# Performance work log

Measured on AMD Instinct MI355X. Metric: run time of the kernel, lower is better.

The kernel has to match this reference:

```python
import jax, jax.numpy as jnp
import numpy as np

B, M, D, S, TOPK = 8, 4096, 512, 128, 64


def setup_inputs() -> dict:
    key = jax.random.key(0)
    ks = jax.random.split(key, 9)
    return {
        "memory": jax.random.normal(ks[0], (B, M, D), jnp.float32),
        "usage": jax.random.uniform(ks[1], (B, M), dtype=jnp.float32),
        "content": jax.random.normal(ks[2], (B, D), jnp.float32),
        "write_strength": jax.random.uniform(ks[3], (B, 1), dtype=jnp.float32),
        "query": jax.random.normal(ks[4], (B, S, D), jnp.float32),
        "key_proj_w": jax.random.normal(ks[5], (D, D), jnp.float32) * 0.02,
        "temporal_table": jax.random.normal(ks[6], (M, D), jnp.float32) * 0.02,
        "usage_decay": jnp.float32(0.99),
        "valid_mask": jax.random.randint(ks[7], (B, M), 0, 2) > 0,
        "write_index": jax.random.randint(ks[8], (B,), 0, M),
        "top_k": TOPK,
    }


def reference(memory, usage, content, write_strength, query, key_proj_w,
              temporal_table, usage_decay, valid_mask, write_index, top_k):
    # ---- write(): soft scatter into the slot selected by write_index ----
    idx = write_index % M                               # [B]
    temporal_emb = temporal_table[idx]                  # [B, D] gather
    content_wt = content + temporal_emb                 # [B, D]
    write_pos = jax.nn.one_hot(idx, M, dtype=memory.dtype)      # [B, M]
    a = write_pos[:, :, None] * write_strength[:, :, None]      # [B, M, 1]
    memory = memory * (1.0 - a) + content_wt[:, None, :] * a    # [B, M, D]
    valid = jnp.logical_or(valid_mask, write_pos > 0)           # [B, M]
    usage = usage * usage_decay + write_pos * write_strength    # [B, M]
    # ---- read(): content-based addressing with top-k masked softmax ----
    keys = jnp.einsum("bmd,ed->bme", memory, key_proj_w)        # Linear, no bias
    scores = jnp.einsum("bsd,bmd->bsm", query, keys) / (D ** 0.5)
    scores = jnp.where(valid[:, None, :], scores, -jnp.inf)
    top_vals = jax.lax.top_k(scores, top_k)[0]                  # [B, S, top_k]
    threshold = top_vals[..., -1:]                              # kth value
    scores = jnp.where(scores < threshold, -jnp.inf, scores)
    attn = jax.nn.softmax(scores, axis=-1)                      # [B, S, M]
    all_invalid = jnp.all(~valid, axis=-1)[:, None, None]
    attn = jnp.where(all_invalid, 0.0, attn)
    retrieved = jnp.einsum("bsm,bmd->bsd", attn, memory)        # [B, S, D]
    return retrieved, attn, usage
```

## Files before the change

### kernel.cpp

```cpp
#include <hip/hip_runtime.h>
#include <hip/hip_bf16.h>
#include <math.h>

#define BB 8
#define MM 4096
#define DD 512
#define SS 128

typedef short s16x8 __attribute__((ext_vector_type(8)));
typedef float f32x4 __attribute__((ext_vector_type(4)));

__device__ __forceinline__ unsigned short f2bf(float x) {
  unsigned u = __float_as_uint(x);
  unsigned r = u + 0x7fffu + ((u >> 16) & 1u);
  return (unsigned short)(r >> 16);
}
__device__ __forceinline__ float bf2f(unsigned short h) {
  return __uint_as_float(((unsigned)h) << 16);
}
__device__ __forceinline__ void split3(float x, unsigned short& s1,
                                       unsigned short& s2, unsigned short& s3) {
  s1 = f2bf(x);
  float r1 = x - bf2f(s1);
  s2 = f2bf(r1);
  float r2 = r1 - bf2f(s2);
  s3 = f2bf(r2);
}

__global__ __launch_bounds__(256) void update_kernel(
    float* __restrict__ memory, const float* __restrict__ usage,
    const float* __restrict__ content, const float* __restrict__ wstr,
    const float* __restrict__ ttab, const float* __restrict__ decay_p,
    const int* __restrict__ widx, float* __restrict__ usage_out) {
  const int b = blockIdx.x;
  int idx = widx[b] % MM; if (idx < 0) idx += MM;
  const float ws = wstr[b];
  const float decay = decay_p[0];
  for (int d = threadIdx.x; d < DD; d += blockDim.x) {
    float cw = content[b * DD + d] + ttab[(size_t)idx * DD + d];
    size_t off = (size_t)b * MM * DD + (size_t)idx * DD + d;
    float old = memory[off];
    memory[off] = old * (1.0f - ws) + cw * ws;
  }
  for (int m = threadIdx.x; m < MM; m += blockDim.x) {
    float u = usage[b * MM + m] * decay;
    if (m == idx) u += ws;
    usage_out[b * MM + m] = u;
  }
}

#define BMq 64
#define BNq 64
#define BKq 32
#define PADq 4

__global__ __launch_bounds__(256) void gemm_nn_qp(
    const float* __restrict__ A, const float* __restrict__ Bw,
    unsigned short* __restrict__ q1, unsigned short* __restrict__ q2,
    unsigned short* __restrict__ q3) {
  __shared__ __align__(16) float As[BKq][BMq + PADq];
  __shared__ __align__(16) float Bs[BKq][BNq + PADq];
  const int tid = threadIdx.x;
  const int tx = tid & 15, ty = tid >> 4;
  const int i0 = blockIdx.y * BMq;
  const int j0 = blockIdx.x * BNq;
  float acc[4][4] = {{0.f}};
  for (int k0 = 0; k0 < DD; k0 += BKq) {
#pragma unroll
    for (int r = 0; r < 2; ++r) {
      int ff = tid + r * 256;
      int row = ff >> 3, kq = ff & 7;
      float4 v = *(const float4*)(A + (size_t)(i0 + row) * DD + k0 + kq * 4);
      As[kq * 4 + 0][row] = v.x; As[kq * 4 + 1][row] = v.y;
      As[kq * 4 + 2][row] = v.z; As[kq * 4 + 3][row] = v.w;
      int kr = ff >> 4, jq = ff & 15;
      float4 w = *(const float4*)(Bw + (size_t)(k0 + kr) * DD + j0 + jq * 4);
      *(float4*)&Bs[kr][jq * 4] = w;
    }
    __syncthreads();
#pragma unroll
    for (int k = 0; k < BKq; ++k) {
      float4 a = *(const float4*)&As[k][ty * 4];
      float4 bb = *(const float4*)&Bs[k][tx * 4];
      float av[4] = {a.x, a.y, a.z, a.w};
      float bv[4] = {bb.x, bb.y, bb.z, bb.w};
#pragma unroll
      for (int i = 0; i < 4; ++i)
#pragma unroll
        for (int j = 0; j < 4; ++j) acc[i][j] += av[i] * bv[j];
    }
    __syncthreads();
  }
#pragma unroll
  for (int i = 0; i < 4; ++i) {
    int row = i0 + ty * 4 + i;
    ushort4 v1, v2, v3;
    split3(acc[i][0], v1.x, v2.x, v3.x);
    split3(acc[i][1], v1.y, v2.y, v3.y);
    split3(acc[i][2], v1.z, v2.z, v3.z);
    split3(acc[i][3], v1.w, v2.w, v3.w);
    *(ushort4*)(q1 + (size_t)row * DD + j0 + tx * 4) = v1;
    *(ushort4*)(q2 + (size_t)row * DD + j0 + tx * 4) = v2;
    *(ushort4*)(q3 + (size_t)row * DD + j0 + tx * 4) = v3;
  }
}

#define LSTR 40

__global__ __launch_bounds__(256, 1) void gemm_scores_mfma(
    const unsigned short* __restrict__ q1_g,
    const unsigned short* __restrict__ q2_g,
    const unsigned short* __restrict__ q3_g,
    const float* __restrict__ mem, float* __restrict__ sc_out) {
  __shared__ __align__(16) unsigned short q1_s[128 * LSTR];
  __shared__ __align__(16) unsigned short q2_s[128 * LSTR];
  __shared__ __align__(16) unsigned short q3_s[128 * LSTR];
  __shared__ __align__(16) unsigned short m1_s[128 * LSTR];
  __shared__ __align__(16) unsigned short m2_s[128 * LSTR];
  __shared__ __align__(16) unsigned short m3_s[128 * LSTR];
  const int tid = threadIdx.x;
  const int b = blockIdx.x & 7;
  const int j0 = (blockIdx.x >> 3) * 128;
  const int wv = tid >> 6, lane = tid & 63;
  const int quad = lane >> 4, r = lane & 15;

  const int qrow0 = tid >> 2, qc = tid & 3;
  const int qrow1 = 64 + (tid >> 2);
  const unsigned short* q1b = q1_g + (size_t)b * SS * DD;
  const unsigned short* q2b = q2_g + (size_t)b * SS * DD;
  const unsigned short* q3b = q3_g + (size_t)b * SS * DD;
  const int mrow = tid >> 3, mk = tid & 7;
  const float* mbase = mem + ((size_t)b * MM + j0) * DD;

  f32x4 acc[2][8];
#pragma unroll
  for (int i = 0; i < 2; ++i)
#pragma unroll
    for (int j = 0; j < 8; ++j)
#pragma unroll
      for (int c = 0; c < 4; ++c) acc[i][j][c] = 0.f;

  uint4 q1r0, q1r1, q2r0, q2r1, q3r0, q3r1;
  float4 mr[4];

  q1r0 = *(const uint4*)(q1b + (size_t)qrow0 * DD + qc * 8);
  q1r1 = *(const uint4*)(q1b + (size_t)qrow1 * DD + qc * 8);
  q2r0 = *(const uint4*)(q2b + (size_t)qrow0 * DD + qc * 8);
  q2r1 = *(const uint4*)(q2b + (size_t)qrow1 * DD + qc * 8);
  q3r0 = *(const uint4*)(q3b + (size_t)qrow0 * DD + qc * 8);
  q3r1 = *(const uint4*)(q3b + (size_t)qrow1 * DD + qc * 8);
#pragma unroll
  for (int i = 0; i < 4; ++i)
    mr[i] = *(const float4*)(mbase + (size_t)(mrow + 32 * i) * DD + mk * 4);

  for (int ks = 0; ks < 16; ++ks) {
    if (ks) __syncthreads();
    *(uint4*)&q1_s[qrow0 * LSTR + qc * 8] = q1r0;
    *(uint4*)&q1_s[qrow1 * LSTR + qc * 8] = q1r1;
    *(uint4*)&q2_s[qrow0 * LSTR + qc * 8] = q2r0;
    *(uint4*)&q2_s[qrow1 * LSTR + qc * 8] = q2r1;
    *(uint4*)&q3_s[qrow0 * LSTR + qc * 8] = q3r0;
    *(uint4*)&q3_s[qrow1 * LSTR + qc * 8] = q3r1;
#pragma unroll
    for (int i = 0; i < 4; ++i) {
      ushort4 v1, v2, v3;
      split3(mr[i].x, v1.x, v2.x, v3.x);
      split3(mr[i].y, v1.y, v2.y, v3.y);
      split3(mr[i].z, v1.z, v2.z, v3.z);
      split3(mr[i].w, v1.w, v2.w, v3.w);
      int row = mrow + 32 * i;
      *(ushort4*)&m1_s[row * LSTR + mk * 4] = v1;
      *(ushort4*)&m2_s[row * LSTR + mk * 4] = v2;
      *(ushort4*)&m3_s[row * LSTR + mk * 4] = v3;
    }
    __syncthreads();
    if (ks < 15) {
      int k0 = (ks + 1) * 32;
      q1r0 = *(const uint4*)(q1b + (size_t)qrow0 * DD + k0 + qc * 8);
      q1r1 = *(const uint4*)(q1b + (size_t)qrow1 * DD + k0 + qc * 8);
      q2r0 = *(const uint4*)(q2b + (size_t)qrow0 * DD + k0 + qc * 8);
      q2r1 = *(const uint4*)(q2b + (size_t)qrow1 * DD + k0 + qc * 8);
      q3r0 = *(const uint4*)(q3b + (size_t)qrow0 * DD + k0 + qc * 8);
      q3r1 = *(const uint4*)(q3b + (size_t)qrow1 * DD + k0 + qc * 8);
#pragma unroll
      for (int i = 0; i < 4; ++i)
        mr[i] = *(const float4*)(mbase + (size_t)(mrow + 32 * i) * DD + k0 + mk * 4);
    }
    s16x8 a1[2], a2[2], a3[2];
#pragma unroll
    for (int st = 0; st < 2; ++st) {
      int arow = wv * 32 + st * 16 + r;
      a1[st] = *(const s16x8*)&q1_s[arow * LSTR + quad * 8];
      a2[st] = *(const s16x8*)&q2_s[arow * LSTR + quad * 8];
      a3[st] = *(const s16x8*)&q3_s[arow * LSTR + quad * 8];
    }
#pragma unroll
    for (int jt = 0; jt < 8; ++jt) {
      int brow = jt * 16 + r;
      s16x8 b1 = *(const s16x8*)&m1_s[brow * LSTR + quad * 8];
      s16x8 b2 = *(const s16x8*)&m2_s[brow * LSTR + quad * 8];
      s16x8 b3 = *(const s16x8*)&m3_s[brow * LSTR + quad * 8];
#pragma unroll
      for (int st = 0; st < 2; ++st) {
        acc[st][jt] = __builtin_amdgcn_mfma_f32_16x16x32_bf16(a1[st], b3, acc[st][jt], 0, 0, 0);
        acc[st][jt] = __builtin_amdgcn_mfma_f32_16x16x32_bf16(a3[st], b1, acc[st][jt], 0, 0, 0);
        acc[st][jt] = __builtin_amdgcn_mfma_f32_16x16x32_bf16(a2[st], b2, acc[st][jt], 0, 0, 0);
        acc[st][jt] = __builtin_amdgcn_mfma_f32_16x16x32_bf16(a1[st], b2, acc[st][jt], 0, 0, 0);
        acc[st][jt] = __builtin_amdgcn_mfma_f32_16x16x32_bf16(a2[st], b1, acc[st][jt], 0, 0, 0);
        acc[st][jt] = __builtin_amdgcn_mfma_f32_16x16x32_bf16(a1[st], b1, acc[st][jt], 0, 0, 0);
      }
    }
  }
  const float scl = 0.04419417382415922f;
  float* C = sc_out + (size_t)b * SS * MM;
#pragma unroll
  for (int st = 0; st < 2; ++st)
#pragma unroll
    for (int jt = 0; jt < 8; ++jt)
#pragma unroll
      for (int reg = 0; reg < 4; ++reg) {
        int srow = wv * 32 + st * 16 + quad * 4 + reg;
        int scol = j0 + jt * 16 + r;
        C[(size_t)srow * MM + scol] = acc[st][jt][reg] * scl;
      }
}

__device__ __forceinline__ unsigned fkey(float f) {
  unsigned u = __float_as_uint(f);
  return (u & 0x80000000u) ? ~u : (u | 0x80000000u);
}
__device__ __forceinline__ float finv(unsigned u) {
  unsigned b = (u & 0x80000000u) ? (u & 0x7fffffffu) : ~u;
  return __uint_as_float(b);
}

__global__ __launch_bounds__(256) void select_kernel(
    const float* __restrict__ scores, const int* __restrict__ vmask,
    const int* __restrict__ widx, const int* __restrict__ topk,
    const float* __restrict__ memory, float* __restrict__ retrieved,
    float* __restrict__ attn) {
  __shared__ float sc[MM];
  __shared__ int kept[MM];
  __shared__ unsigned histw[4 * 256];
  __shared__ float red[256];
  __shared__ unsigned sh_pref;
  __shared__ int sh_k, sh_nkept;
  __shared__ float sh_zinv;

  const int tid = threadIdx.x;
  const int s = blockIdx.x, b = blockIdx.y;
  int wi = widx[b] % MM; if (wi < 0) wi += MM;
  const float4* srow4 = (const float4*)(scores + ((size_t)b * SS + s) * MM);
  const int4* vrow4 = (const int4*)(vmask + (size_t)b * MM);
  unsigned* hw = histw + (tid >> 6) * 256;

  if (tid == 0) { sh_pref = 0u; sh_nkept = 0; sh_k = topk[0]; }
  for (int i = tid; i < 1024; i += 256) histw[i] = 0u;
  __syncthreads();

  float lmax = -INFINITY;
  for (int m4 = tid; m4 < MM / 4; m4 += 256) {
    float4 v = srow4[m4];
    int4 mk = vrow4[m4];
    int mb = m4 * 4;
    if (!(mk.x || mb + 0 == wi)) v.x = -INFINITY;
    if (!(mk.y || mb + 1 == wi)) v.y = -INFINITY;
    if (!(mk.z || mb + 2 == wi)) v.z = -INFINITY;
    if (!(mk.w || mb + 3 == wi)) v.w = -INFINITY;
    ((float4*)sc)[m4] = v;
    lmax = fmaxf(lmax, fmaxf(fmaxf(v.x, v.y), fmaxf(v.z, v.w)));
    atomicAdd(&hw[fkey(v.x) >> 24], 1u);
    atomicAdd(&hw[fkey(v.y) >> 24], 1u);
    atomicAdd(&hw[fkey(v.z) >> 24], 1u);
    atomicAdd(&hw[fkey(v.w) >> 24], 1u);
  }
  red[tid] = lmax;
  __syncthreads();
#pragma unroll
  for (int off = 128; off > 0; off >>= 1) {
    if (tid < off) red[tid] = fmaxf(red[tid], red[tid + off]);
    __syncthreads();
  }
  const float maxv = red[0];

  for (int pass = 0; pass < 4; ++pass) {
    const int shift = 24 - pass * 8;
    if (pass > 0) {
      const unsigned pref = sh_pref;
      const unsigned hmask = 0xFFFFFFFFu << (shift + 8);
      for (int i = tid; i < 1024; i += 256) histw[i] = 0u;
      __syncthreads();
      for (int m = tid; m < MM; m += 256) {
        unsigned u = fkey(sc[m]);
        if ((u & hmask) == pref) atomicAdd(&hw[(u >> shift) & 0xFFu], 1u);
      }
      __syncthreads();
    }
    if (tid < 64) {
      const int l = tid;
      unsigned h0 = histw[l * 4 + 0] + histw[256 + l * 4 + 0] + histw[512 + l * 4 + 0] + histw[768 + l * 4 + 0];
      unsigned h1 = histw[l * 4 + 1] + histw[256 + l * 4 + 1] + histw[512 + l * 4 + 1] + histw[768 + l * 4 + 1];
      unsigned h2 = histw[l * 4 + 2] + histw[256 + l * 4 + 2] + histw[512 + l * 4 + 2] + histw[768 + l * 4 + 2];
      unsigned h3 = histw[l * 4 + 3] + histw[256 + l * 4 + 3] + histw[512 + l * 4 + 3] + histw[768 + l * 4 + 3];
      unsigned lsum = h0 + h1 + h2 + h3;
      unsigned g = lsum;
#pragma unroll
      for (int off = 1; off < 64; off <<= 1) {
        unsigned t = __shfl_down(g, off, 64);
        if (l + off < 64) g += t;
      }
      unsigned above = g - lsum;
      unsigned suf3 = h3 + above;
      unsigned suf2 = h2 + suf3;
      unsigned suf1 = h1 + suf2;
      unsigned suf0 = h0 + suf1;
      const unsigned kk = (unsigned)sh_k;
      const unsigned prefc = sh_pref;
      unsigned ge, geN;
      ge = suf0; geN = suf1;
      if (ge >= kk && geN < kk) { sh_pref = prefc | ((unsigned)(4 * l + 0) << shift); sh_k = (int)(kk - geN); }
      ge = suf1; geN = suf2;
      if (ge >= kk && geN < kk) { sh_pref = prefc | ((unsigned)(4 * l + 1) << shift); sh_k = (int)(kk - geN); }
      ge = suf2; geN = suf3;
      if (ge >= kk && geN < kk) { sh_pref = prefc | ((unsigned)(4 * l + 2) << shift); sh_k = (int)(kk - geN); }
      ge = suf3; geN = above;
      if (ge >= kk && geN < kk) { sh_pref = prefc | ((unsigned)(4 * l + 3) << shift); sh_k = (int)(kk - geN); }
    }
    __syncthreads();
  }
  const float thr = finv(sh_pref);

  float lz = 0.f;
  for (int m4 = tid; m4 < MM / 4; m4 += 256) {
    float4 v = ((float4*)sc)[m4];
    v.x = (v.x >= thr) ? __expf(v.x - maxv) : 0.f;
    v.y = (v.y >= thr) ? __expf(v.y - maxv) : 0.f;
    v.z = (v.z >= thr) ? __expf(v.z - maxv) : 0.f;
    v.w = (v.w >= thr) ? __expf(v.w - maxv) : 0.f;
    ((float4*)sc)[m4] = v;
    lz += v.x + v.y + v.z + v.w;
  }
  red[tid] = lz;
  __syncthreads();
#pragma unroll
  for (int off = 128; off > 0; off >>= 1) {
    if (tid < off) red[tid] += red[tid + off];
    __syncthreads();
  }
  if (tid == 0) sh_zinv = 1.0f / red[0];
  __syncthreads();
  const float zinv = sh_zinv;

  float4* arow4 = (float4*)(attn + ((size_t)b * SS + s) * MM);
  for (int m4 = tid; m4 < MM / 4; m4 += 256) {
    float4 p = ((float4*)sc)[m4];
    float4 o = make_float4(p.x * zinv, p.y * zinv, p.z * zinv, p.w * zinv);
    arow4[m4] = o;
    int mb = m4 * 4;
    if (p.x > 0.f) kept[atomicAdd(&sh_nkept, 1)] = mb + 0;
    if (p.y > 0.f) kept[atomicAdd(&sh_nkept, 1)] = mb + 1;
    if (p.z > 0.f) kept[atomicAdd(&sh_nkept, 1)] = mb + 2;
    if (p.w > 0.f) kept[atomicAdd(&sh_nkept, 1)] = mb + 3;
  }
  __syncthreads();
  const int nk = sh_nkept;

  float a0 = 0.f, a1 = 0.f;
  const float* mb_ = memory + (size_t)b * MM * DD;
  int i = 0;
  for (; i + 4 <= nk; i += 4) {
    int m0 = kept[i], m1 = kept[i + 1], m2 = kept[i + 2], m3 = kept[i + 3];
    float p0 = sc[m0], p1 = sc[m1], p2 = sc[m2], p3 = sc[m3];
    const float* r0 = mb_ + (size_t)m0 * DD;
    const float* r1 = mb_ + (size_t)m1 * DD;
    const float* r2 = mb_ + (size_t)m2 * DD;
    const float* r3 = mb_ + (size_t)m3 * DD;
    float v0a = r0[tid], v0b = r0[tid + 256];
    float v1a = r1[tid], v1b = r1[tid + 256];
    float v2a = r2[tid], v2b = r2[tid + 256];
    float v3a = r3[tid], v3b = r3[tid + 256];
    a0 += p0 * v0a + p1 * v1a + p2 * v2a + p3 * v3a;
    a1 += p0 * v0b + p1 * v1b + p2 * v2b + p3 * v3b;
  }
  for (; i < nk; ++i) {
    int m = kept[i];
    float p = sc[m];
    const float* mr = mb_ + (size_t)m * DD;
    a0 += p * mr[tid];
    a1 += p * mr[tid + 256];
  }
  float* rrow = retrieved + ((size_t)b * SS + s) * DD;
  rrow[tid] = a0 * zinv;
  rrow[tid + 256] = a1 * zinv;
}

extern "C" void kernel_launch(void* const* d_in, const int* in_sizes, int n_in,
                              void* d_out, int out_size, void* d_ws,
                              size_t ws_size, hipStream_t stream) {
  float* memory = (float*)d_in[0];
  const float* usage = (const float*)d_in[1];
  const float* content = (const float*)d_in[2];
  const float* wstr = (const float*)d_in[3];
  const float* query = (const float*)d_in[4];
  const float* W = (const float*)d_in[5];
  const float* ttab = (const float*)d_in[6];
  const float* decay = (const float*)d_in[7];
  const int* vmask = (const int*)d_in[8];
  const int* widx = (const int*)d_in[9];
  const int* topk = (const int*)d_in[10];

  float* out = (float*)d_out;
  float* retrieved = out;
  float* attn = out + (size_t)BB * SS * DD;
  float* usage_out = attn + (size_t)BB * SS * MM;

  const size_t qsz = (size_t)BB * SS * DD;
  float* scores = (float*)d_ws;
  unsigned short* q1 = (unsigned short*)(scores + (size_t)BB * SS * MM);
  unsigned short* q2 = q1 + qsz;
  unsigned short* q3;
  size_t need3 = (size_t)BB * SS * MM * 4 + 3 * qsz * 2;
  if (ws_size >= need3) {
    q3 = q2 + qsz;
  } else {
    q3 = (unsigned short*)(attn + (size_t)BB * SS * MM) - qsz;
  }

  update_kernel<<<BB, 256, 0, stream>>>(memory, usage, content, wstr, ttab,
                                        decay, widx, usage_out);
  gemm_nn_qp<<<dim3(DD / BNq, (BB * SS) / BMq), 256, 0, stream>>>(query, W, q1,
                                                                  q2, q3);
  gemm_scores_mfma<<<dim3((MM / 128) * BB), 256, 0, stream>>>(q1, q2, q3,
                                                              memory, scores);
  select_kernel<<<dim3(SS, BB), 256, 0, stream>>>(scores, vmask, widx, topk,
                                                  memory, retrieved, attn);
}
```

Before: 203.4 us.

## Switch split-precision GEMMs from 3-way bf16 to 2-way fp16 MFMA

Replaces the 3-term bf16 split (6 MFMAs per tile) with a 2-term fp16 hi/lo split (3 MFMAs) in the scores GEMM. The query-projection GEMM moves from scalar FP32 FMA to fp16 MFMA with the same split. The scores kernel now uses 64-column tiles, reads query fragments straight from global memory into registers instead of staging them in LDS, and allows two blocks per CU. This cuts MFMA count and LDS traffic, but fp16 has a narrower exponent range and coarser split precision, which could perturb the top-k ordering.

```diff
diff --git a/kernel.cpp b/kernel.cpp
--- a/kernel.cpp
+++ b/kernel.cpp
@@ -7,24 +7,17 @@
 #define DD 512
 #define SS 128
 
-typedef short s16x8 __attribute__((ext_vector_type(8)));
+typedef _Float16 f16;
+typedef _Float16 f16x4 __attribute__((ext_vector_type(4)));
+typedef _Float16 f16x8 __attribute__((ext_vector_type(8)));
 typedef float f32x4 __attribute__((ext_vector_type(4)));
 
-__device__ __forceinline__ unsigned short f2bf(float x) {
-  unsigned u = __float_as_uint(x);
-  unsigned r = u + 0x7fffu + ((u >> 16) & 1u);
-  return (unsigned short)(r >> 16);
-}
-__device__ __forceinline__ float bf2f(unsigned short h) {
-  return __uint_as_float(((unsigned)h) << 16);
-}
-__device__ __forceinline__ void split3(float x, unsigned short& s1,
-                                       unsigned short& s2, unsigned short& s3) {
-  s1 = f2bf(x);
-  float r1 = x - bf2f(s1);
-  s2 = f2bf(r1);
-  float r2 = r1 - bf2f(s2);
-  s3 = f2bf(r2);
+struct f16pair { f16 h; f16 l; };
+__device__ __forceinline__ f16pair split2(float x) {
+  f16pair p;
+  p.h = (f16)x;
+  p.l = (f16)(x - (float)p.h);
+  return p;
 }
 
 __global__ __launch_bounds__(256) void update_kernel(
@@ -49,166 +42,197 @@
   }
 }
 
-#define BMq 64
-#define BNq 64
-#define BKq 32
-#define PADq 4
-
-__global__ __launch_bounds__(256) void gemm_nn_qp(
-    const float* __restrict__ A, const float* __restrict__ Bw,
-    unsigned short* __restrict__ q1, unsigned short* __restrict__ q2,
-    unsigned short* __restrict__ q3) {
-  __shared__ __align__(16) float As[BKq][BMq + PADq];
-  __shared__ __align__(16) float Bs[BKq][BNq + PADq];
+#define QLSTR 40
+
+__global__ __launch_bounds__(256) void gemm_qp_mfma(
+    const float* __restrict__ query, const float* __restrict__ W,
+    f16* __restrict__ q1, f16* __restrict__ q2) {
+  __shared__ __align__(16) f16 A1s[64 * QLSTR];
+  __shared__ __align__(16) f16 A2s[64 * QLSTR];
+  __shared__ __align__(16) f16 B1s[64 * QLSTR];
+  __shared__ __align__(16) f16 B2s[64 * QLSTR];
   const int tid = threadIdx.x;
-  const int tx = tid & 15, ty = tid >> 4;
-  const int i0 = blockIdx.y * BMq;
-  const int j0 = blockIdx.x * BNq;
-  float acc[4][4] = {{0.f}};
-  for (int k0 = 0; k0 < DD; k0 += BKq) {
-#pragma unroll
-    for (int r = 0; r < 2; ++r) {
-      int ff = tid + r * 256;
-      int row = ff >> 3, kq = ff & 7;
-      float4 v = *(const float4*)(A + (size_t)(i0 + row) * DD + k0 + kq * 4);
-      As[kq * 4 + 0][row] = v.x; As[kq * 4 + 1][row] = v.y;
-      As[kq * 4 + 2][row] = v.z; As[kq * 4 + 3][row] = v.w;
-      int kr = ff >> 4, jq = ff & 15;
-      float4 w = *(const float4*)(Bw + (size_t)(k0 + kr) * DD + j0 + jq * 4);
-      *(float4*)&Bs[kr][jq * 4] = w;
-    }
-    __syncthreads();
-#pragma unroll
-    for (int k = 0; k < BKq; ++k) {
-      float4 a = *(const float4*)&As[k][ty * 4];
-      float4 bb = *(const float4*)&Bs[k][tx * 4];
-      float av[4] = {a.x, a.y, a.z, a.w};
-      float bv[4] = {bb.x, bb.y, bb.z, bb.w};
-#pragma unroll
-      for (int i = 0; i < 4; ++i)
-#pragma unroll
-        for (int j = 0; j < 4; ++j) acc[i][j] += av[i] * bv[j];
-    }
-    __syncthreads();
-  }
-#pragma unroll
-  for (int i = 0; i < 4; ++i) {
-    int row = i0 + ty * 4 + i;
-    ushort4 v1, v2, v3;
-    split3(acc[i][0], v1.x, v2.x, v3.x);
-    split3(acc[i][1], v1.y, v2.y, v3.y);
-    split3(acc[i][2], v1.z, v2.z, v3.z);
-    split3(acc[i][3], v1.w, v2.w, v3.w);
-    *(ushort4*)(q1 + (size_t)row * DD + j0 + tx * 4) = v1;
-    *(ushort4*)(q2 + (size_t)row * DD + j0 + tx * 4) = v2;
-    *(ushort4*)(q3 + (size_t)row * DD + j0 + tx * 4) = v3;
-  }
-}
-
-#define LSTR 40
-
-__global__ __launch_bounds__(256, 1) void gemm_scores_mfma(
-    const unsigned short* __restrict__ q1_g,
-    const unsigned short* __restrict__ q2_g,
-    const unsigned short* __restrict__ q3_g,
-    const float* __restrict__ mem, float* __restrict__ sc_out) {
-  __shared__ __align__(16) unsigned short q1_s[128 * LSTR];
-  __shared__ __align__(16) unsigned short q2_s[128 * LSTR];
-  __shared__ __align__(16) unsigned short q3_s[128 * LSTR];
-  __shared__ __align__(16) unsigned short m1_s[128 * LSTR];
-  __shared__ __align__(16) unsigned short m2_s[128 * LSTR];
-  __shared__ __align__(16) unsigned short m3_s[128 * LSTR];
-  const int tid = threadIdx.x;
-  const int b = blockIdx.x & 7;
-  const int j0 = (blockIdx.x >> 3) * 128;
+  const int n0 = blockIdx.x * 64;
+  const int r0 = blockIdx.y * 64;
   const int wv = tid >> 6, lane = tid & 63;
-  const int quad = lane >> 4, r = lane & 15;
-
-  const int qrow0 = tid >> 2, qc = tid & 3;
-  const int qrow1 = 64 + (tid >> 2);
-  const unsigned short* q1b = q1_g + (size_t)b * SS * DD;
-  const unsigned short* q2b = q2_g + (size_t)b * SS * DD;
-  const unsigned short* q3b = q3_g + (size_t)b * SS * DD;
-  const int mrow = tid >> 3, mk = tid & 7;
-  const float* mbase = mem + ((size_t)b * MM + j0) * DD;
-
-  f32x4 acc[2][8];
+  const int quad = lane >> 4, rr = lane & 15;
+  const int wr = wv & 1, wc = wv >> 1;
+
+  const int arow = tid >> 3, ak = tid & 7;
+  const int bkr = tid >> 4, bnq = tid & 15;
+
+  f32x4 acc[2][2];
 #pragma unroll
   for (int i = 0; i < 2; ++i)
 #pragma unroll
-    for (int j = 0; j < 8; ++j)
+    for (int j = 0; j < 2; ++j)
 #pragma unroll
       for (int c = 0; c < 4; ++c) acc[i][j][c] = 0.f;
 
-  uint4 q1r0, q1r1, q2r0, q2r1, q3r0, q3r1;
-  float4 mr[4];
-
-  q1r0 = *(const uint4*)(q1b + (size_t)qrow0 * DD + qc * 8);
-  q1r1 = *(const uint4*)(q1b + (size_t)qrow1 * DD + qc * 8);
-  q2r0 = *(const uint4*)(q2b + (size_t)qrow0 * DD + qc * 8);
-  q2r1 = *(const uint4*)(q2b + (size_t)qrow1 * DD + qc * 8);
-  q3r0 = *(const uint4*)(q3b + (size_t)qrow0 * DD + qc * 8);
-  q3r1 = *(const uint4*)(q3b + (size_t)qrow1 * DD + qc * 8);
-#pragma unroll
-  for (int i = 0; i < 4; ++i)
-    mr[i] = *(const float4*)(mbase + (size_t)(mrow + 32 * i) * DD + mk * 4);
+  float4 ar0, ar1, br0, br1;
+  ar0 = *(const float4*)(query + (size_t)(r0 + arow) * DD + ak * 4);
+  ar1 = *(const float4*)(query + (size_t)(r0 + arow + 32) * DD + ak * 4);
+  br0 = *(const float4*)(W + (size_t)bkr * DD + n0 + bnq * 4);
+  br1 = *(const float4*)(W + (size_t)(bkr + 16) * DD + n0 + bnq * 4);
 
   for (int ks = 0; ks < 16; ++ks) {
     if (ks) __syncthreads();
-    *(uint4*)&q1_s[qrow0 * LSTR + qc * 8] = q1r0;
-    *(uint4*)&q1_s[qrow1 * LSTR + qc * 8] = q1r1;
-    *(uint4*)&q2_s[qrow0 * LSTR + qc * 8] = q2r0;
-    *(uint4*)&q2_s[qrow1 * LSTR + qc * 8] = q2r1;
-    *(uint4*)&q3_s[qrow0 * LSTR + qc * 8] = q3r0;
-    *(uint4*)&q3_s[qrow1 * LSTR + qc * 8] = q3r1;
-#pragma unroll
-    for (int i = 0; i < 4; ++i) {
-      ushort4 v1, v2, v3;
-      split3(mr[i].x, v1.x, v2.x, v3.x);
-      split3(mr[i].y, v1.y, v2.y, v3.y);
-      split3(mr[i].z, v1.z, v2.z, v3.z);
-      split3(mr[i].w, v1.w, v2.w, v3.w);
-      int row = mrow + 32 * i;
-      *(ushort4*)&m1_s[row * LSTR + mk * 4] = v1;
-      *(ushort4*)&m2_s[row * LSTR + mk * 4] = v2;
-      *(ushort4*)&m3_s[row * LSTR + mk * 4] = v3;
+    {
+      f16x4 h, l;
+      f16pair p;
+      p = split2(ar0.x); h[0] = p.h; l[0] = p.l;
+      p = split2(ar0.y); h[1] = p.h; l[1] = p.l;
+      p = split2(ar0.z); h[2] = p.h; l[2] = p.l;
+      p = split2(ar0.w); h[3] = p.h; l[3] = p.l;
+      *(f16x4*)&A1s[arow * QLSTR + ak * 4] = h;
+      *(f16x4*)&A2s[arow * QLSTR + ak * 4] = l;
+      p = split2(ar1.x); h[0] = p.h; l[0] = p.l;
+      p = split2(ar1.y); h[1] = p.h; l[1] = p.l;
+      p = split2(ar1.z); h[2] = p.h; l[2] = p.l;
+      p = split2(ar1.w); h[3] = p.h; l[3] = p.l;
+      *(f16x4*)&A1s[(arow + 32) * QLSTR + ak * 4] = h;
+      *(f16x4*)&A2s[(arow + 32) * QLSTR + ak * 4] = l;
+      float wv4[4] = {br0.x, br0.y, br0.z, br0.w};
+#pragma unroll
+      for (int i = 0; i < 4; ++i) {
+        f16pair q = split2(wv4[i]);
+        B1s[(bnq * 4 + i) * QLSTR + bkr] = q.h;
+        B2s[(bnq * 4 + i) * QLSTR + bkr] = q.l;
+      }
+      float wv5[4] = {br1.x, br1.y, br1.z, br1.w};
+#pragma unroll
+      for (int i = 0; i < 4; ++i) {
+        f16pair q = split2(wv5[i]);
+        B1s[(bnq * 4 + i) * QLSTR + bkr + 16] = q.h;
+        B2s[(bnq * 4 + i) * QLSTR + bkr + 16] = q.l;
+      }
     }
     __syncthreads();
     if (ks < 15) {
       int k0 = (ks + 1) * 32;
-      q1r0 = *(const uint4*)(q1b + (size_t)qrow0 * DD + k0 + qc * 8);
-      q1r1 = *(const uint4*)(q1b + (size_t)qrow1 * DD + k0 + qc * 8);
-      q2r0 = *(const uint4*)(q2b + (size_t)qrow0 * DD + k0 + qc * 8);
-      q2r1 = *(const uint4*)(q2b + (size_t)qrow1 * DD + k0 + qc * 8);
-      q3r0 = *(const uint4*)(q3b + (size_t)qrow0 * DD + k0 + qc * 8);
-      q3r1 = *(const uint4*)(q3b + (size_t)qrow1 * DD + k0 + qc * 8);
-#pragma unroll
-      for (int i = 0; i < 4; ++i)
-        mr[i] = *(const float4*)(mbase + (size_t)(mrow + 32 * i) * DD + k0 + mk * 4);
-    }
-    s16x8 a1[2], a2[2], a3[2];
+      ar0 = *(const float4*)(query + (size_t)(r0 + arow) * DD + k0 + ak * 4);
+      ar1 = *(const float4*)(query + (size_t)(r0 + arow + 32) * DD + k0 + ak * 4);
+      br0 = *(const float4*)(W + (size_t)(k0 + bkr) * DD + n0 + bnq * 4);
+      br1 = *(const float4*)(W + (size_t)(k0 + bkr + 16) * DD + n0 + bnq * 4);
+    }
+    f16x8 a1[2], a2[2];
 #pragma unroll
     for (int st = 0; st < 2; ++st) {
-      int arow = wv * 32 + st * 16 + r;
-      a1[st] = *(const s16x8*)&q1_s[arow * LSTR + quad * 8];
-      a2[st] = *(const s16x8*)&q2_s[arow * LSTR + quad * 8];
-      a3[st] = *(const s16x8*)&q3_s[arow * LSTR + quad * 8];
-    }
-#pragma unroll
-    for (int jt = 0; jt < 8; ++jt) {
-      int brow = jt * 16 + r;
-      s16x8 b1 = *(const s16x8*)&m1_s[brow * LSTR + quad * 8];
-      s16x8 b2 = *(const s16x8*)&m2_s[brow * LSTR + quad * 8];
-      s16x8 b3 = *(const s16x8*)&m3_s[brow * LSTR + quad * 8];
+      int row = wr * 32 + st * 16 + rr;
+      a1[st] = *(const f16x8*)&A1s[row * QLSTR + quad * 8];
+      a2[st] = *(const f16x8*)&A2s[row * QLSTR + quad * 8];
+    }
+#pragma unroll
+    for (int ct = 0; ct < 2; ++ct) {
+      int col = wc * 32 + ct * 16 + rr;
+      f16x8 b1 = *(const f16x8*)&B1s[col * QLSTR + quad * 8];
+      f16x8 b2 = *(const f16x8*)&B2s[col * QLSTR + quad * 8];
 #pragma unroll
       for (int st = 0; st < 2; ++st) {
-        acc[st][jt] = __builtin_amdgcn_mfma_f32_16x16x32_bf16(a1[st], b3, acc[st][jt], 0, 0, 0);
-        acc[st][jt] = __builtin_amdgcn_mfma_f32_16x16x32_bf16(a3[st], b1, acc[st][jt], 0, 0, 0);
-        acc[st][jt] = __builtin_amdgcn_mfma_f32_16x16x32_bf16(a2[st], b2, acc[st][jt], 0, 0, 0);
-        acc[st][jt] = __builtin_amdgcn_mfma_f32_16x16x32_bf16(a1[st], b2, acc[st][jt], 0, 0, 0);
-        acc[st][jt] = __builtin_amdgcn_mfma_f32_16x16x32_bf16(a2[st], b1, acc[st][jt], 0, 0, 0);
-        acc[st][jt] = __builtin_amdgcn_mfma_f32_16x16x32_bf16(a1[st], b1, acc[st][jt], 0, 0, 0);
-      }
+        acc[st][ct] = __builtin_amdgcn_mfma_f32_16x16x32_f16(a1[st], b2, acc[st][ct], 0, 0, 0);
+        acc[st][ct] = __builtin_amdgcn_mfma_f32_16x16x32_f16(a2[st], b1, acc[st][ct], 0, 0, 0);
+        acc[st][ct] = __builtin_amdgcn_mfma_f32_16x16x32_f16(a1[st], b1, acc[st][ct], 0, 0, 0);
+      }
+    }
+  }
+#pragma unroll
+  for (int st = 0; st < 2; ++st)
+#pragma unroll
+    for (int ct = 0; ct < 2; ++ct)
+#pragma unroll
+      for (int reg = 0; reg < 4; ++reg) {
+        int row = r0 + wr * 32 + st * 16 + quad * 4 + reg;
+        int col = n0 + wc * 32 + ct * 16 + rr;
+        f16pair p = split2(acc[st][ct][reg]);
+        q1[(size_t)row * DD + col] = p.h;
+        q2[(size_t)row * DD + col] = p.l;
+      }
+}
+
+#define LSTR 40
+
+__global__ __launch_bounds__(256, 2) void gemm_scores_mfma(
+    const f16* __restrict__ q1_g, const f16* __restrict__ q2_g,
+    const float* __restrict__ mem, float* __restrict__ sc_out) {
+  __shared__ __align__(16) f16 m1_s[64 * LSTR];
+  __shared__ __align__(16) f16 m2_s[64 * LSTR];
+  const int tid = threadIdx.x;
+  const int b = blockIdx.x & 7;
+  const int j0 = (blockIdx.x >> 3) * 64;
+  const int wv = tid >> 6, lane = tid & 63;
+  const int quad = lane >> 4, rr = lane & 15;
+
+  const f16* q1b = q1_g + (size_t)b * SS * DD;
+  const f16* q2b = q2_g + (size_t)b * SS * DD;
+  const int mrow = tid >> 3, mk = tid & 7;
+  const float* mbase = mem + ((size_t)b * MM + j0) * DD;
+
+  f32x4 acc[2][4];
+#pragma unroll
+  for (int i = 0; i < 2; ++i)
+#pragma unroll
+    for (int j = 0; j < 4; ++j)
+#pragma unroll
+      for (int c = 0; c < 4; ++c) acc[i][j][c] = 0.f;
+
+  float4 mr0, mr1;
+  f16x8 a1c[2], a2c[2], a1n[2], a2n[2];
+
+  mr0 = *(const float4*)(mbase + (size_t)mrow * DD + mk * 4);
+  mr1 = *(const float4*)(mbase + (size_t)(mrow + 32) * DD + mk * 4);
+#pragma unroll
+  for (int st = 0; st < 2; ++st) {
+    int srow = wv * 32 + st * 16 + rr;
+    a1c[st] = *(const f16x8*)(q1b + (size_t)srow * DD + quad * 8);
+    a2c[st] = *(const f16x8*)(q2b + (size_t)srow * DD + quad * 8);
+  }
+
+  for (int ks = 0; ks < 16; ++ks) {
+    if (ks) __syncthreads();
+    {
+      f16x4 h, l;
+      f16pair p;
+      p = split2(mr0.x); h[0] = p.h; l[0] = p.l;
+      p = split2(mr0.y); h[1] = p.h; l[1] = p.l;
+      p = split2(mr0.z); h[2] = p.h; l[2] = p.l;
+      p = split2(mr0.w); h[3] = p.h; l[3] = p.l;
+      *(f16x4*)&m1_s[mrow * LSTR + mk * 4] = h;
+      *(f16x4*)&m2_s[mrow * LSTR + mk * 4] = l;
+      p = split2(mr1.x); h[0] = p.h; l[0] = p.l;
+      p = split2(mr1.y); h[1] = p.h; l[1] = p.l;
+      p = split2(mr1.z); h[2] = p.h; l[2] = p.l;
+      p = split2(mr1.w); h[3] = p.h; l[3] = p.l;
+      *(f16x4*)&m1_s[(mrow + 32) * LSTR + mk * 4] = h;
+      *(f16x4*)&m2_s[(mrow + 32) * LSTR + mk * 4] = l;
+    }
+    __syncthreads();
+    if (ks < 15) {
+      int k0 = (ks + 1) * 32;
+      mr0 = *(const float4*)(mbase + (size_t)mrow * DD + k0 + mk * 4);
+      mr1 = *(const float4*)(mbase + (size_t)(mrow + 32) * DD + k0 + mk * 4);
+#pragma unroll
+      for (int st = 0; st < 2; ++st) {
+        int srow = wv * 32 + st * 16 + rr;
+        a1n[st] = *(const f16x8*)(q1b + (size_t)srow * DD + k0 + quad * 8);
+        a2n[st] = *(const f16x8*)(q2b + (size_t)srow * DD + k0 + quad * 8);
+      }
+    }
+#pragma unroll
+    for (int jt = 0; jt < 4; ++jt) {
+      int brow = jt * 16 + rr;
+      f16x8 b1 = *(const f16x8*)&m1_s[brow * LSTR + quad * 8];
+      f16x8 b2 = *(const f16x8*)&m2_s[brow * LSTR + quad * 8];
+#pragma unroll
+      for (int st = 0; st < 2; ++st) {
+        acc[st][jt] = __builtin_amdgcn_mfma_f32_16x16x32_f16(a1c[st], b2, acc[st][jt], 0, 0, 0);
+        acc[st][jt] = __builtin_amdgcn_mfma_f32_16x16x32_f16(a2c[st], b1, acc[st][jt], 0, 0, 0);
+        acc[st][jt] = __builtin_amdgcn_mfma_f32_16x16x32_f16(a1c[st], b1, acc[st][jt], 0, 0, 0);
+      }
+    }
+#pragma unroll
+    for (int st = 0; st < 2; ++st) {
+      a1c[st] = a1n[st];
+      a2c[st] = a2n[st];
     }
   }
   const float scl = 0.04419417382415922f;
@@ -216,11 +240,11 @@
 #pragma unroll
   for (int st = 0; st < 2; ++st)
 #pragma unroll
-    for (int jt = 0; jt < 8; ++jt)
+    for (int jt = 0; jt < 4; ++jt)
 #pragma unroll
       for (int reg = 0; reg < 4; ++reg) {
         int srow = wv * 32 + st * 16 + quad * 4 + reg;
-        int scol = j0 + jt * 16 + r;
+        int scol = j0 + jt * 16 + rr;
         C[(size_t)srow * MM + scol] = acc[st][jt][reg] * scl;
       }
 }
@@ -416,22 +440,23 @@
 
   const size_t qsz = (size_t)BB * SS * DD;
   float* scores = (float*)d_ws;
-  unsigned short* q1 = (unsigned short*)(scores + (size_t)BB * SS * MM);
-  unsigned short* q2 = q1 + qsz;
-  unsigned short* q3;
-  size_t need3 = (size_t)BB * SS * MM * 4 + 3 * qsz * 2;
-  if (ws_size >= need3) {
-    q3 = q2 + qsz;
+  f16* q1;
+  f16* q2;
+  size_t need = (size_t)BB * SS * MM * 4 + 2 * qsz * 2;
+  if (ws_size >= need) {
+    q1 = (f16*)(scores + (size_t)BB * SS * MM);
+    q2 = q1 + qsz;
   } else {
-    q3 = (unsigned short*)(attn + (size_t)BB * SS * MM) - qsz;
+    q2 = (f16*)(attn + (size_t)BB * SS * MM) - qsz;
+    q1 = q2 - qsz;
   }
 
   update_kernel<<<BB, 256, 0, stream>>>(memory, usage, content, wstr, ttab,
                                         decay, widx, usage_out);
-  gemm_nn_qp<<<dim3(DD / BNq, (BB * SS) / BMq), 256, 0, stream>>>(query, W, q1,
-                                                                  q2, q3);
-  gemm_scores_mfma<<<dim3((MM / 128) * BB), 256, 0, stream>>>(q1, q2, q3,
-                                                              memory, scores);
+  gemm_qp_mfma<<<dim3(DD / 64, (BB * SS) / 64), 256, 0, stream>>>(query, W, q1,
+                                                                  q2);
+  gemm_scores_mfma<<<dim3((MM / 64) * BB), 256, 0, stream>>>(q1, q2, memory,
+                                                             scores);
   select_kernel<<<dim3(SS, BB), 256, 0, stream>>>(scores, vmask, widx, topk,
                                                   memory, retrieved, attn);
 }
```

Measured after the change: 201.9 us. No clear change (-0.7%).
